# Kernel tuning notes

Hardware: AMD Instinct MI355X
Metric: run time of the kernel (lower is better)

Reference implementation:

```python
import jax, jax.numpy as jnp
import numpy as np

SX, SY, C, K = 256, 256, 3, 15
DD, DT, SIGMA = 5, 0.2, 0.65
C0 = tuple(i % C for i in range(K))
C1 = tuple(tuple(i for i in range(K) if i % C == c) for c in range(C))
MA = DD - SIGMA  # flow magnitude bound


def _sobel(A):
    # A: (X, Y, c) -> (X, Y, 2, c); matches jsp.signal.convolve2d(..., mode='same')
    kx = jnp.array([[1., 0., -1.], [2., 0., -2.], [1., 0., -1.]], dtype=A.dtype)
    ky = kx.T
    # convolve2d flips the kernel; emulate true convolution by correlating with rot180 kernels
    kern = jnp.stack([jnp.rot90(ky, 2), jnp.rot90(kx, 2)])[:, None]  # (2,1,3,3): [grad_y, grad_x]
    x = jnp.transpose(A, (2, 0, 1))[:, None]                          # (c,1,X,Y)
    out = jax.lax.conv_general_dilated(x, kern, (1, 1), 'SAME')       # (c,2,X,Y)
    return jnp.transpose(out, (2, 3, 1, 0))                           # (X,Y,2,c)


def _reintegration(A, P, F):
    # Reintegration tracking, has_hidden=True, border='wall', mix='softmax'
    xs, ys = jnp.meshgrid(jnp.arange(SX), jnp.arange(SY))
    pos = (jnp.dstack((ys, xs)) + .5).astype(A.dtype)     # (X,Y,2) cell centers (row, col)
    mus = pos[..., None] + jnp.clip(DT * F, -MA, MA)      # (X,Y,2,C) target centers
    mus = jnp.clip(mus, SIGMA, SX - SIGMA)                # wall border
    shifts = jnp.array([(dx, dy) for dx in range(-DD, DD + 1) for dy in range(-DD, DD + 1)])
    cap = min(1., 2 * SIGMA)

    def step(sft):
        sh = (sft[0], sft[1])
        Ar = jnp.roll(A, sh, axis=(0, 1))
        Pr = jnp.roll(P, sh, axis=(0, 1))
        mur = jnp.roll(mus, sh, axis=(0, 1))
        dpmu = jnp.abs(pos[..., None] - mur)              # (X,Y,2,C)
        sz = .5 - dpmu + SIGMA
        area = jnp.prod(jnp.clip(sz, 0., cap), axis=2) / (4 * SIGMA ** 2)  # (X,Y,C)
        return Ar * area, Pr

    nA, nP = jax.vmap(step)(shifts)                       # (N,X,Y,C), (N,X,Y,K)
    expnA = jnp.exp(nA.sum(-1, keepdims=True)) - 1.       # softmax mix rule
    newA = nA.sum(0)
    newP = (nP * expnA).sum(0) / (expnA.sum(0) + 1e-10)
    return newA, newP


def _forward(A, P, fK_real, fK_imag, m, s):
    fK = fK_real + 1j * fK_imag                           # (X,Y,K) kernel FFTs
    fA = jnp.fft.fft2(A, axes=(0, 1))                     # (X,Y,C)
    fAk = jnp.take(fA, jnp.array(C0), axis=2)             # (X,Y,K) per-kernel source channel
    U = jnp.real(jnp.fft.ifft2(fK * fAk, axes=(0, 1)))    # (X,Y,K)
    U = (2. * jnp.exp(-((U - m) ** 2) / (2. * s ** 2)) - 1.) * P  # growth(U,m,s)*P
    U = jnp.dstack([U[:, :, C1[c]].sum(-1) for c in range(C)])    # (X,Y,C)
    F = _sobel(U)                                         # (X,Y,2,C)
    Cg = _sobel(A.sum(-1, keepdims=True))                 # (X,Y,2,1)
    alpha = jnp.clip((A[:, :, None, :] / 2.) ** 2, 0., 1.)
    F = jnp.clip(F * (1. - alpha) - Cg * alpha, -MA, MA)
    return _reintegration(A, P, F)


def setup_inputs() -> dict:
    key = jax.random.key(0)
    kA, kP, kr, km, ks, ka, kb, kw = jax.random.split(key, 8)
    A = jax.random.uniform(kA, (SX, SY, C), dtype=jnp.float32)
    P = jax.random.uniform(kP, (SX, SY, K), dtype=jnp.float32)
    R = 15.0
    r = jax.random.uniform(kr, (K,), minval=.2, maxval=1.)
    m = jax.random.uniform(km, (K,), minval=.05, maxval=.5, dtype=jnp.float32)
    s = jax.random.uniform(ks, (K,), minval=.001, maxval=.18, dtype=jnp.float32)
    a = jax.random.uniform(ka, (K, 3))
    b = jax.random.uniform(kb, (K, 3), minval=.001, maxval=1.)
    w = jax.random.uniform(kw, (K, 3), minval=.01, maxval=.5)
    mid = SX // 2
    D = jnp.linalg.norm(jnp.mgrid[-mid:mid, -mid:mid], axis=0)[..., None] / ((R + 15.) * r)  # (X,Y,K)
    Kk = jax.nn.sigmoid(-(D - 1.) * 10.) * (b * jnp.exp(-((D[..., None] - a) / w) ** 2)).sum(-1)
    nK = Kk / Kk.sum((0, 1), keepdims=True)
    fK = jnp.fft.fft2(jnp.fft.fftshift(nK, axes=(0, 1)), axes=(0, 1))
    return {"A": A, "P": P,
            "fK_real": jnp.real(fK).astype(jnp.float32),
            "fK_imag": jnp.imag(fK).astype(jnp.float32),
            "m": m, "s": s}


def reference(A, P, fK_real, fK_imag, m, s):
    return _forward(A, P, fK_real, fK_imag, m, s)
```

## Files before the change

kernel.cpp:

```cpp
#include <hip/hip_runtime.h>


#define XY  65536
#define NC  3
#define NK  15
#define WPAD 260

__device__ __forceinline__ float2 cmul(float2 a, float2 b) {
  return make_float2(a.x * b.x - a.y * b.y, a.x * b.y + a.y * b.x);
}

__device__ __forceinline__ void fft256_lds(float2* b0, float2* b1, int t, float sign) {
  float2* src = b0;
  float2* dst = b1;
#pragma unroll
  for (int stage = 0; stage < 4; ++stage) {
    __syncthreads();
    const int Ns = 1 << (2 * stage);
    float2 v0 = src[t];
    float2 v1 = src[t + 64];
    float2 v2 = src[t + 128];
    float2 v3 = src[t + 192];
    const int jm = t & (Ns - 1);
    float ang = sign * 6.283185307179586f * (float)jm / (float)(Ns * 4);
    float sn, cs;
    __sincosf(ang, &sn, &cs);
    float2 w1 = make_float2(cs, sn);
    float2 w2 = cmul(w1, w1);
    float2 w3 = cmul(w2, w1);
    v1 = cmul(v1, w1);
    v2 = cmul(v2, w2);
    v3 = cmul(v3, w3);
    float2 a0 = make_float2(v0.x + v2.x, v0.y + v2.y);
    float2 a1 = make_float2(v0.x - v2.x, v0.y - v2.y);
    float2 a2 = make_float2(v1.x + v3.x, v1.y + v3.y);
    float2 a3 = make_float2(v1.x - v3.x, v1.y - v3.y);
    float2 ia3 = make_float2(-sign * a3.y, sign * a3.x);
    const int idxD = ((t >> (2 * stage)) << (2 * stage)) * 4 + jm;
    dst[idxD]          = make_float2(a0.x + a2.x, a0.y + a2.y);
    dst[idxD + Ns]     = make_float2(a1.x + ia3.x, a1.y + ia3.y);
    dst[idxD + 2 * Ns] = make_float2(a0.x - a2.x, a0.y - a2.y);
    dst[idxD + 3 * Ns] = make_float2(a1.x - ia3.x, a1.y - ia3.y);
    float2* tmp = src; src = dst; dst = tmp;
  }
  __syncthreads();
}

__global__ __launch_bounds__(256) void k_prep(const float* __restrict__ A,
                                              const float* __restrict__ P,
                                              float* __restrict__ Aplan,
                                              float* __restrict__ Asum,
                                              float* __restrict__ Pplan) {
  const int b = blockIdx.x * 256 + threadIdx.x;
  float a0 = A[b * 3 + 0], a1 = A[b * 3 + 1], a2 = A[b * 3 + 2];
  Aplan[0 * XY + b] = a0;
  Aplan[1 * XY + b] = a1;
  Aplan[2 * XY + b] = a2;
  Asum[b] = a0 + a1 + a2;
#pragma unroll
  for (int k = 0; k < NK; ++k) Pplan[k * XY + b] = P[b * NK + k];
}

__global__ __launch_bounds__(256) void k_rowfft(const float* __restrict__ Aplan,
                                                float2* __restrict__ RF) {
  __shared__ float2 lds0[4 * WPAD], lds1[4 * WPAD];
  const int tid = threadIdx.x;
  const int w = tid >> 6, lane = tid & 63;
  const int c = blockIdx.x >> 6;
  const int x = ((blockIdx.x & 63) << 2) + w;
  float2* b0 = lds0 + w * WPAD;
  float2* b1 = lds1 + w * WPAD;
  const float* src = Aplan + c * XY + x * 256;
#pragma unroll
  for (int r = 0; r < 4; ++r) {
    int y = lane + 64 * r;
    b0[y] = make_float2(src[y], 0.0f);
  }
  fft256_lds(b0, b1, lane, -1.0f);
#pragma unroll
  for (int r = 0; r < 4; ++r) {
    int y = lane + 64 * r;
    RF[(c * 256 + x) * 256 + y] = b0[y];
  }
}

__global__ __launch_bounds__(512, 1) void k_colfft(const float* __restrict__ fKr,
                                                   const float* __restrict__ fKi,
                                                   const float2* __restrict__ RF,
                                                   float2* __restrict__ T2) {
  __shared__ float2 lds0[8 * WPAD];
  __shared__ float2 lds1[8 * WPAD];
  const int tid = threadIdx.x;
  const int k = blockIdx.x >> 5;
  const int y0 = (blockIdx.x & 31) << 3;
  const int c = k % 3;

  {
    const int q = tid & 3;
#pragma unroll
    for (int r = 0; r < 2; ++r) {
      const int x = (tid >> 2) + (r << 7);
      const float4* src = (const float4*)(RF + (c * XY + x * 256 + y0));
      float4 v = src[q];
      lds0[(2 * q) * WPAD + x]     = make_float2(v.x, v.y);
      lds0[(2 * q + 1) * WPAD + x] = make_float2(v.z, v.w);
    }
  }

  const int w = tid >> 6, lane = tid & 63;
  float2* b0 = lds0 + w * WPAD;
  float2* b1 = lds1 + w * WPAD;
  fft256_lds(b0, b1, lane, -1.0f);

  const int y = y0 + w;
  float2 fa[4];
#pragma unroll
  for (int r = 0; r < 4; ++r) fa[r] = b0[lane + 64 * r];
#pragma unroll
  for (int r = 0; r < 4; ++r) {
    const int x = lane + 64 * r;
    const int fi = (x * 256 + y) * NK + k;
    float2 Kv = make_float2(fKr[fi], fKi[fi]);
    b0[x] = cmul(Kv, fa[r]);
  }
  fft256_lds(b0, b1, lane, 1.0f);

  {
    const int q = tid & 3;
#pragma unroll
    for (int r = 0; r < 2; ++r) {
      const int x = (tid >> 2) + (r << 7);
      float2 v0 = lds0[(2 * q) * WPAD + x];
      float2 v1 = lds0[(2 * q + 1) * WPAD + x];
      float4* dst = (float4*)(T2 + (k * XY + x * 256 + y0));
      dst[q] = make_float4(v0.x, v0.y, v1.x, v1.y);
    }
  }
}

__global__ __launch_bounds__(320, 1) void k_irowfft_growth(const float2* __restrict__ T2,
                                                           const float* __restrict__ Pplan,
                                                           const float* __restrict__ m,
                                                           const float* __restrict__ s,
                                                           float* __restrict__ Ucol) {
  __shared__ float2 lds0[5 * WPAD];
  __shared__ float2 lds1[5 * WPAD];
  __shared__ float accs[5 * WPAD];
  const int tid = threadIdx.x;
  const int x = blockIdx.x & 255;
  const int c = blockIdx.x >> 8;
  const int j = tid >> 6, lane = tid & 63;
  const int k = c + 3 * j;

  float2* b0 = lds0 + j * WPAD;
  float2* b1 = lds1 + j * WPAD;
  const float2* src = T2 + (k * XY + x * 256);
#pragma unroll
  for (int r = 0; r < 4; ++r) {
    int y = lane + 64 * r;
    b0[y] = src[y];
  }
  fft256_lds(b0, b1, lane, 1.0f);

  const float mk = m[k];
  const float sk = s[k];
  const float inv2s2 = 0.5f / (sk * sk);
  const float* pk = Pplan + k * XY + x * 256;
#pragma unroll
  for (int r = 0; r < 4; ++r) {
    int y = lane + 64 * r;
    float U = b0[y].x * (1.0f / 65536.0f);
    float d = U - mk;
    float g = 2.0f * __expf(-d * d * inv2s2) - 1.0f;
    accs[j * WPAD + y] = g * pk[y];
  }
  __syncthreads();
  if (tid < 256) {
    float sum = 0.f;
#pragma unroll
    for (int j2 = 0; j2 < 5; ++j2) sum += accs[j2 * WPAD + tid];
    Ucol[c * XY + x * 256 + tid] = sum;
  }
}

__global__ __launch_bounds__(256) void k_flow(const float* __restrict__ Aplan,
                                              const float* __restrict__ Asum,
                                              const float* __restrict__ Ucol,
                                              float* __restrict__ Fplan) {
  const int idx = blockIdx.x * 256 + threadIdx.x;
  const int x = idx >> 8;
  const int y = idx & 255;
  const float MA = 4.35f;

  float u[3][3][3];
  float as[3][3];
#pragma unroll
  for (int di = -1; di <= 1; ++di) {
#pragma unroll
    for (int dj = -1; dj <= 1; ++dj) {
      int xi = x + di, yj = y + dj;
      bool inb = ((unsigned)xi < 256u) && ((unsigned)yj < 256u);
      float a0 = 0.f, a1 = 0.f, a2 = 0.f, asv = 0.f;
      if (inb) {
        int b = xi * 256 + yj;
        a0 = Ucol[0 * XY + b];
        a1 = Ucol[1 * XY + b];
        a2 = Ucol[2 * XY + b];
        asv = Asum[b];
      }
      u[0][di + 1][dj + 1] = a0;
      u[1][di + 1][dj + 1] = a1;
      u[2][di + 1][dj + 1] = a2;
      as[di + 1][dj + 1] = asv;
    }
  }
  float cg0 = (as[2][0] + 2.f * as[2][1] + as[2][2]) -
              (as[0][0] + 2.f * as[0][1] + as[0][2]);
  float cg1 = (as[0][2] + 2.f * as[1][2] + as[2][2]) -
              (as[0][0] + 2.f * as[1][0] + as[2][0]);
  const int b = x * 256 + y;
#pragma unroll
  for (int c = 0; c < NC; ++c) {
    float f0 = (u[c][2][0] + 2.f * u[c][2][1] + u[c][2][2]) -
               (u[c][0][0] + 2.f * u[c][0][1] + u[c][0][2]);
    float f1 = (u[c][0][2] + 2.f * u[c][1][2] + u[c][2][2]) -
               (u[c][0][0] + 2.f * u[c][1][0] + u[c][2][0]);
    float ah = Aplan[c * XY + b] * 0.5f;
    float al = fminf(ah * ah, 1.0f);
    f0 = fminf(fmaxf(f0 * (1.f - al) - cg0 * al, -MA), MA);
    f1 = fminf(fmaxf(f1 * (1.f - al) - cg1 * al, -MA), MA);
    Fplan[(0 * 3 + c) * XY + b] = f0;
    Fplan[(1 * 3 + c) * XY + b] = f1;
  }
}

__global__ __launch_bounds__(256) void k_reint(const float* __restrict__ Aplan,
                                               const float* __restrict__ Pplan,
                                               const float* __restrict__ Fplan,
                                               float* __restrict__ outA,
                                               float* __restrict__ outP) {
  const int idx = blockIdx.x * 256 + threadIdx.x;
  const int x = idx >> 8;
  const int y = idx & 255;
  const float SIGMA = 0.65f;
  const float INV4S2 = 1.0f / (4.0f * 0.65f * 0.65f);
  const float DT = 0.2f;
  const float px = x + 0.5f;
  const float py = y + 0.5f;

  float accA[3] = {0.f, 0.f, 0.f};
  float accP[15];
#pragma unroll
  for (int k = 0; k < NK; ++k) accP[k] = 0.f;
  float esum = 0.f;

  for (int dx = -2; dx <= 2; ++dx) {
    for (int dy = -2; dy <= 2; ++dy) {
      const int sx = (x - dx) & 255;
      const int sy = (y - dy) & 255;
      const int sb = sx * 256 + sy;
      const float spx = sx + 0.5f;
      const float spy = sy + 0.5f;
      float sumnA = 0.f;
      float nAc[3];
#pragma unroll
      for (int c = 0; c < NC; ++c) {
        float f0 = Fplan[(0 * 3 + c) * XY + sb];
        float f1 = Fplan[(1 * 3 + c) * XY + sb];
        float mu0 = fminf(fmaxf(spx + DT * f0, SIGMA), 256.f - SIGMA);
        float mu1 = fminf(fmaxf(spy + DT * f1, SIGMA), 256.f - SIGMA);
        float sz0 = 0.5f - fabsf(px - mu0) + SIGMA;
        float sz1 = 0.5f - fabsf(py - mu1) + SIGMA;
        sz0 = fminf(fmaxf(sz0, 0.f), 1.f);
        sz1 = fminf(fmaxf(sz1, 0.f), 1.f);
        float area = sz0 * sz1 * INV4S2;
        float na = Aplan[c * XY + sb] * area;
        nAc[c] = na;
        sumnA += na;
      }
      float e = __expf(sumnA) - 1.0f;
      accA[0] += nAc[0];
      accA[1] += nAc[1];
      accA[2] += nAc[2];
      esum += e;
#pragma unroll
      for (int k = 0; k < NK; ++k) accP[k] += Pplan[k * XY + sb] * e;
    }
  }
  const int b = x * 256 + y;
#pragma unroll
  for (int c = 0; c < NC; ++c) outA[b * NC + c] = accA[c];
  const float inv = 1.0f / (esum + 1e-10f);
#pragma unroll
  for (int k = 0; k < NK; ++k) outP[b * NK + k] = accP[k] * inv;
}

extern "C" void kernel_launch(void* const* d_in, const int* in_sizes, int n_in,
                              void* d_out, int out_size, void* d_ws, size_t ws_size,
                              hipStream_t stream) {
  const float* A   = (const float*)d_in[0];
  const float* P   = (const float*)d_in[1];
  const float* fKr = (const float*)d_in[2];
  const float* fKi = (const float*)d_in[3];
  const float* m   = (const float*)d_in[4];
  const float* s   = (const float*)d_in[5];

  float* ws = (float*)d_ws;
  float2* RF    = (float2*)ws;
  float2* T2    = RF + NC * XY;
  float*  Ucol  = (float*)(T2 + NK * XY);
  float*  Fplan = Ucol + NC * XY;
  float*  Aplan = Fplan + 6 * XY;
  float*  Asum  = Aplan + NC * XY;
  float*  Pplan = Asum + XY;

  float* outA = (float*)d_out;
  float* outP = outA + NC * XY;

  k_prep<<<256, 256, 0, stream>>>(A, P, Aplan, Asum, Pplan);
  k_rowfft<<<NC * 64, 256, 0, stream>>>(Aplan, RF);
  k_colfft<<<NK * 32, 512, 0, stream>>>(fKr, fKi, RF, T2);
  k_irowfft_growth<<<NC * 256, 320, 0, stream>>>(T2, Pplan, m, s, Ucol);
  k_flow<<<256, 256, 0, stream>>>(Aplan, Asum, Ucol, Fplan);
  k_reint<<<256, 256, 0, stream>>>(Aplan, Pplan, Fplan, outA, outP);
}
```

Measured before the change: 111.3 us.

## Fuse flow and reintegration kernels with LDS tiles and wave-skip of empty shifts

Merges the Sobel flow kernel into the reintegration kernel. Each block computes flow and A values for an 8x32 tile plus halo into shared memory, then gathers neighbours from LDS instead of global memory. It skips P accumulation for shifts whose mass is zero across the whole wavefront, and stages outputs in LDS for coalesced interleaved stores. This removes one launch and the global round trip of the flow field, at the cost of recomputing flow on halo cells and using more LDS.

```diff
diff --git a/kernel.cpp b/kernel.cpp
--- a/kernel.cpp
+++ b/kernel.cpp
@@ -183,90 +183,112 @@
   }
 }
 
-__global__ __launch_bounds__(256) void k_flow(const float* __restrict__ Aplan,
-                                              const float* __restrict__ Asum,
-                                              const float* __restrict__ Ucol,
-                                              float* __restrict__ Fplan) {
-  const int idx = blockIdx.x * 256 + threadIdx.x;
-  const int x = idx >> 8;
-  const int y = idx & 255;
+#define UROW 14
+#define UCOLW 38
+#define FROW 12
+#define FCOLW 36
+#define LPAD 40
+__global__ __launch_bounds__(256, 2) void k_flow_reint(const float* __restrict__ Aplan,
+                                                       const float* __restrict__ Asum,
+                                                       const float* __restrict__ Ucol,
+                                                       const float* __restrict__ Pplan,
+                                                       float* __restrict__ outA,
+                                                       float* __restrict__ outP) {
+  __shared__ float smem[3 * UROW * LPAD + UROW * LPAD + 6 * FROW * LPAD + 3 * FROW * LPAD];
+  float* Uc = smem;
+  float* As = Uc + 3 * UROW * LPAD;
+  float* Ft = As + UROW * LPAD;
+  float* At = Ft + 6 * FROW * LPAD;
+  float* PoutS = smem;
+  float* AoutS = smem + 8 * 480;
+
+  const int tid = threadIdx.x;
+  const int x0 = (blockIdx.x >> 3) << 3;
+  const int y0 = (blockIdx.x & 7) << 5;
+
+  for (int i = tid; i < UROW * UCOLW; i += 256) {
+    const int lx = i / UCOLW, ly = i - lx * UCOLW;
+    const int gx = (x0 - 3 + lx) & 255;
+    const int gy = (y0 - 3 + ly) & 255;
+    const int g = gx * 256 + gy;
+    Uc[0 * UROW * LPAD + lx * LPAD + ly] = Ucol[0 * XY + g];
+    Uc[1 * UROW * LPAD + lx * LPAD + ly] = Ucol[1 * XY + g];
+    Uc[2 * UROW * LPAD + lx * LPAD + ly] = Ucol[2 * XY + g];
+    As[lx * LPAD + ly] = Asum[g];
+  }
+  __syncthreads();
+
   const float MA = 4.35f;
-
-  float u[3][3][3];
-  float as[3][3];
-#pragma unroll
-  for (int di = -1; di <= 1; ++di) {
-#pragma unroll
-    for (int dj = -1; dj <= 1; ++dj) {
-      int xi = x + di, yj = y + dj;
-      bool inb = ((unsigned)xi < 256u) && ((unsigned)yj < 256u);
-      float a0 = 0.f, a1 = 0.f, a2 = 0.f, asv = 0.f;
-      if (inb) {
-        int b = xi * 256 + yj;
-        a0 = Ucol[0 * XY + b];
-        a1 = Ucol[1 * XY + b];
-        a2 = Ucol[2 * XY + b];
-        asv = Asum[b];
-      }
-      u[0][di + 1][dj + 1] = a0;
-      u[1][di + 1][dj + 1] = a1;
-      u[2][di + 1][dj + 1] = a2;
-      as[di + 1][dj + 1] = asv;
+  for (int i = tid; i < FROW * FCOLW; i += 256) {
+    const int j = i / FCOLW, l = i - j * FCOLW;
+    const int wx = (x0 - 2 + j) & 255;
+    const int wy = (y0 - 2 + l) & 255;
+    const bool xm = (wx != 0), xp = (wx != 255);
+    const bool ym = (wy != 0), yp = (wy != 255);
+    float a00 = (xm && ym) ? As[(j) * LPAD + l] : 0.f;
+    float a01 = xm ? As[(j) * LPAD + l + 1] : 0.f;
+    float a02 = (xm && yp) ? As[(j) * LPAD + l + 2] : 0.f;
+    float a10 = ym ? As[(j + 1) * LPAD + l] : 0.f;
+    float a12 = yp ? As[(j + 1) * LPAD + l + 2] : 0.f;
+    float a20 = (xp && ym) ? As[(j + 2) * LPAD + l] : 0.f;
+    float a21 = xp ? As[(j + 2) * LPAD + l + 1] : 0.f;
+    float a22 = (xp && yp) ? As[(j + 2) * LPAD + l + 2] : 0.f;
+    float cg0 = (a20 + 2.f * a21 + a22) - (a00 + 2.f * a01 + a02);
+    float cg1 = (a02 + 2.f * a12 + a22) - (a00 + 2.f * a10 + a20);
+    const int wb = wx * 256 + wy;
+#pragma unroll
+    for (int c = 0; c < NC; ++c) {
+      const float* up = Uc + c * UROW * LPAD;
+      float u00 = (xm && ym) ? up[(j) * LPAD + l] : 0.f;
+      float u01 = xm ? up[(j) * LPAD + l + 1] : 0.f;
+      float u02 = (xm && yp) ? up[(j) * LPAD + l + 2] : 0.f;
+      float u10 = ym ? up[(j + 1) * LPAD + l] : 0.f;
+      float u12 = yp ? up[(j + 1) * LPAD + l + 2] : 0.f;
+      float u20 = (xp && ym) ? up[(j + 2) * LPAD + l] : 0.f;
+      float u21 = xp ? up[(j + 2) * LPAD + l + 1] : 0.f;
+      float u22 = (xp && yp) ? up[(j + 2) * LPAD + l + 2] : 0.f;
+      float f0 = (u20 + 2.f * u21 + u22) - (u00 + 2.f * u01 + u02);
+      float f1 = (u02 + 2.f * u12 + u22) - (u00 + 2.f * u10 + u20);
+      float av = Aplan[c * XY + wb];
+      float ah = av * 0.5f;
+      float al = fminf(ah * ah, 1.0f);
+      f0 = fminf(fmaxf(f0 * (1.f - al) - cg0 * al, -MA), MA);
+      f1 = fminf(fmaxf(f1 * (1.f - al) - cg1 * al, -MA), MA);
+      Ft[(0 * 3 + c) * FROW * LPAD + j * LPAD + l] = f0;
+      Ft[(1 * 3 + c) * FROW * LPAD + j * LPAD + l] = f1;
+      At[c * FROW * LPAD + j * LPAD + l] = av;
     }
   }
-  float cg0 = (as[2][0] + 2.f * as[2][1] + as[2][2]) -
-              (as[0][0] + 2.f * as[0][1] + as[0][2]);
-  float cg1 = (as[0][2] + 2.f * as[1][2] + as[2][2]) -
-              (as[0][0] + 2.f * as[1][0] + as[2][0]);
-  const int b = x * 256 + y;
-#pragma unroll
-  for (int c = 0; c < NC; ++c) {
-    float f0 = (u[c][2][0] + 2.f * u[c][2][1] + u[c][2][2]) -
-               (u[c][0][0] + 2.f * u[c][0][1] + u[c][0][2]);
-    float f1 = (u[c][0][2] + 2.f * u[c][1][2] + u[c][2][2]) -
-               (u[c][0][0] + 2.f * u[c][1][0] + u[c][2][0]);
-    float ah = Aplan[c * XY + b] * 0.5f;
-    float al = fminf(ah * ah, 1.0f);
-    f0 = fminf(fmaxf(f0 * (1.f - al) - cg0 * al, -MA), MA);
-    f1 = fminf(fmaxf(f1 * (1.f - al) - cg1 * al, -MA), MA);
-    Fplan[(0 * 3 + c) * XY + b] = f0;
-    Fplan[(1 * 3 + c) * XY + b] = f1;
-  }
-}
-
-__global__ __launch_bounds__(256) void k_reint(const float* __restrict__ Aplan,
-                                               const float* __restrict__ Pplan,
-                                               const float* __restrict__ Fplan,
-                                               float* __restrict__ outA,
-                                               float* __restrict__ outP) {
-  const int idx = blockIdx.x * 256 + threadIdx.x;
-  const int x = idx >> 8;
-  const int y = idx & 255;
+  __syncthreads();
+
+  const int tr = tid >> 5, tcol = tid & 31;
+  const int tx = x0 + tr, ty = y0 + tcol;
   const float SIGMA = 0.65f;
   const float INV4S2 = 1.0f / (4.0f * 0.65f * 0.65f);
   const float DT = 0.2f;
-  const float px = x + 0.5f;
-  const float py = y + 0.5f;
+  const float px = tx + 0.5f;
+  const float py = ty + 0.5f;
 
   float accA[3] = {0.f, 0.f, 0.f};
-  float accP[15];
+  float accP[NK];
 #pragma unroll
   for (int k = 0; k < NK; ++k) accP[k] = 0.f;
   float esum = 0.f;
 
   for (int dx = -2; dx <= 2; ++dx) {
     for (int dy = -2; dy <= 2; ++dy) {
-      const int sx = (x - dx) & 255;
-      const int sy = (y - dy) & 255;
-      const int sb = sx * 256 + sy;
+      const int j = tr - dx + 2;
+      const int l = tcol - dy + 2;
+      const int sx = (tx - dx) & 255;
+      const int sy = (ty - dy) & 255;
       const float spx = sx + 0.5f;
       const float spy = sy + 0.5f;
       float sumnA = 0.f;
       float nAc[3];
 #pragma unroll
       for (int c = 0; c < NC; ++c) {
-        float f0 = Fplan[(0 * 3 + c) * XY + sb];
-        float f1 = Fplan[(1 * 3 + c) * XY + sb];
+        float f0 = Ft[(0 * 3 + c) * FROW * LPAD + j * LPAD + l];
+        float f1 = Ft[(1 * 3 + c) * FROW * LPAD + j * LPAD + l];
         float mu0 = fminf(fmaxf(spx + DT * f0, SIGMA), 256.f - SIGMA);
         float mu1 = fminf(fmaxf(spy + DT * f1, SIGMA), 256.f - SIGMA);
         float sz0 = 0.5f - fabsf(px - mu0) + SIGMA;
@@ -274,25 +296,38 @@
         sz0 = fminf(fmaxf(sz0, 0.f), 1.f);
         sz1 = fminf(fmaxf(sz1, 0.f), 1.f);
         float area = sz0 * sz1 * INV4S2;
-        float na = Aplan[c * XY + sb] * area;
+        float na = At[c * FROW * LPAD + j * LPAD + l] * area;
         nAc[c] = na;
         sumnA += na;
       }
-      float e = __expf(sumnA) - 1.0f;
-      accA[0] += nAc[0];
-      accA[1] += nAc[1];
-      accA[2] += nAc[2];
-      esum += e;
-#pragma unroll
-      for (int k = 0; k < NK; ++k) accP[k] += Pplan[k * XY + sb] * e;
+      if (__any(sumnA != 0.f)) {
+        float e = __expf(sumnA) - 1.0f;
+        accA[0] += nAc[0];
+        accA[1] += nAc[1];
+        accA[2] += nAc[2];
+        esum += e;
+        const int sb = sx * 256 + sy;
+#pragma unroll
+        for (int k = 0; k < NK; ++k) accP[k] += Pplan[k * XY + sb] * e;
+      }
     }
   }
-  const int b = x * 256 + y;
-#pragma unroll
-  for (int c = 0; c < NC; ++c) outA[b * NC + c] = accA[c];
   const float inv = 1.0f / (esum + 1e-10f);
-#pragma unroll
-  for (int k = 0; k < NK; ++k) outP[b * NK + k] = accP[k] * inv;
+
+  __syncthreads();
+#pragma unroll
+  for (int c = 0; c < NC; ++c) AoutS[tr * 96 + tcol * 3 + c] = accA[c];
+#pragma unroll
+  for (int k = 0; k < NK; ++k) PoutS[tr * 480 + tcol * 15 + k] = accP[k] * inv;
+  __syncthreads();
+  for (int i = tid; i < 8 * 96; i += 256) {
+    const int row = i / 96, off = i - row * 96;
+    outA[((x0 + row) * 256 + y0) * 3 + off] = AoutS[i];
+  }
+  for (int i = tid; i < 8 * 480; i += 256) {
+    const int row = i / 480, off = i - row * 480;
+    outP[((x0 + row) * 256 + y0) * NK + off] = PoutS[i];
+  }
 }
 
 extern "C" void kernel_launch(void* const* d_in, const int* in_sizes, int n_in,
@@ -309,8 +344,7 @@
   float2* RF    = (float2*)ws;
   float2* T2    = RF + NC * XY;
   float*  Ucol  = (float*)(T2 + NK * XY);
-  float*  Fplan = Ucol + NC * XY;
-  float*  Aplan = Fplan + 6 * XY;
+  float*  Aplan = Ucol + NC * XY;
   float*  Asum  = Aplan + NC * XY;
   float*  Pplan = Asum + XY;
 
@@ -321,6 +355,5 @@
   k_rowfft<<<NC * 64, 256, 0, stream>>>(Aplan, RF);
   k_colfft<<<NK * 32, 512, 0, stream>>>(fKr, fKi, RF, T2);
   k_irowfft_growth<<<NC * 256, 320, 0, stream>>>(T2, Pplan, m, s, Ucol);
-  k_flow<<<256, 256, 0, stream>>>(Aplan, Asum, Ucol, Fplan);
-  k_reint<<<256, 256, 0, stream>>>(Aplan, Pplan, Fplan, outA, outP);
-}
+  k_flow_reint<<<256, 256, 0, stream>>>(Aplan, Asum, Ucol, Pplan, outA, outP);
+}
```

New measurement: 114.6 us. 2.9% more time.
